# Kernel tuning notes

Hardware: AMD Instinct MI355X
Metric: run time of the kernel (lower is better)

## Reference

```python
import jax, jax.numpy as jnp
import numpy as np

V, D, H, L, S, B, FF, MAXLEN = 50257, 768, 12, 12, 1024, 4, 3072, 1024
HD = D // H
EPS = 1e-5


def layernorm(x, w, b):
    m = jnp.mean(x, axis=-1, keepdims=True)
    v = jnp.mean(jnp.square(x - m), axis=-1, keepdims=True)
    return (x - m) * jax.lax.rsqrt(v + EPS) * w + b


def setup_inputs() -> dict:
    key = jax.random.key(0)
    ks = jax.random.split(key, 8)
    std = 0.02
    return {
        "tokens": jax.random.randint(ks[0], (B, S), 0, V, dtype=jnp.int32),
        "wte": std * jax.random.normal(ks[1], (V, D), jnp.float32),
        "wpe": std * jax.random.normal(ks[2], (1, MAXLEN, D), jnp.float32),
        "ln1_w": jnp.ones((L, D), jnp.float32),
        "ln1_b": jnp.zeros((L, D), jnp.float32),
        "ln2_w": jnp.ones((L, D), jnp.float32),
        "ln2_b": jnp.zeros((L, D), jnp.float32),
        "W_exp": std * jax.random.normal(ks[3], (L, D, 3 * D), jnp.float32),
        "b_exp": jnp.zeros((L, 3 * D), jnp.float32),
        "W_o": std * jax.random.normal(ks[4], (L, D, D), jnp.float32),
        "b_o": jnp.zeros((L, D), jnp.float32),
        "W_ff1": std * jax.random.normal(ks[5], (L, D, FF), jnp.float32),
        "b_ff1": jnp.zeros((L, FF), jnp.float32),
        "W_ff2": std * jax.random.normal(ks[6], (L, FF, D), jnp.float32),
        "b_ff2": jnp.zeros((L, D), jnp.float32),
    }


def reference(tokens, wte, wpe, ln1_w, ln1_b, ln2_w, ln2_b,
              W_exp, b_exp, W_o, b_o, W_ff1, b_ff1, W_ff2, b_ff2):
    Bc, Sc = tokens.shape
    x = wte[tokens] + wpe[:, :Sc, :]                      # [B,S,D]
    mask = jnp.tril(jnp.ones((Sc, Sc), bool))             # causal (past=None)
    scale = 1.0 / jnp.sqrt(jnp.float32(HD))
    presents = []
    for l in range(L):
        h = layernorm(x, ln1_w[l], ln1_b[l])
        qkv = h @ W_exp[l] + b_exp[l]                     # [B,S,3D]
        q, k, v = jnp.split(qkv, 3, axis=-1)
        q = q.reshape(Bc, Sc, H, HD)
        k = k.reshape(Bc, Sc, H, HD)
        v = v.reshape(Bc, Sc, H, HD)
        presents.append(jnp.stack([k, v]))                # [2,B,S,H,HD]
        score = jnp.einsum('bqhd,bkhd->bhqk', q, k)
        score = jnp.where(mask, score, jnp.float32(-1e20))
        attn = jax.nn.softmax(score * scale, axis=-1)     # mask applied BEFORE scaling, as in source
        a = jnp.einsum('bhqk,bkhd->bqhd', attn, v).reshape(Bc, Sc, D)
        a = a @ W_o[l] + b_o[l]
        add = layernorm(a + x, ln2_w[l], ln2_b[l])        # LN2 on residual sum (GPT2-variant in source)
        ff = jax.nn.gelu(add @ W_ff1[l] + b_ff1[l], approximate=False)
        ff = ff @ W_ff2[l] + b_ff2[l]
        x = ff + add
    return x, jnp.stack(presents)                         # [L,2,B,S,H,HD]
```

## Files before the change

### kernel.cpp

```cpp
#include <hip/hip_runtime.h>
#include <hip/hip_bf16.h>
#include <math.h>

#define Bc 4
#define Sc 1024
#define Dc 768
#define Hc 12
#define Lc 12
#define FFc 3072
#define Mtot (Bc*Sc)

typedef __bf16 bf16x8 __attribute__((ext_vector_type(8)));
typedef float f32x4 __attribute__((ext_vector_type(4)));

__device__ __forceinline__ void gload_lds16(const void* g, void* l) {
    __builtin_amdgcn_global_load_lds((const __attribute__((address_space(1))) void*)g,
                                     (__attribute__((address_space(3))) void*)l, 16, 0, 0);
}

__global__ __launch_bounds__(256) void embed_kernel(const int* __restrict__ tokens,
                                                    const float* __restrict__ wte,
                                                    const float* __restrict__ wpe,
                                                    float* __restrict__ x) {
    int row = blockIdx.x;
    int s = row & (Sc - 1);
    int tok = tokens[row];
    const float* wt = wte + (size_t)tok * Dc;
    const float* wp = wpe + (size_t)s * Dc;
    float* xr = x + (size_t)row * Dc;
#pragma unroll
    for (int k = 0; k < 3; ++k) {
        int d = threadIdx.x + k * 256;
        xr[d] = wt[d] + wp[d];
    }
}

__global__ __launch_bounds__(256) void transpose_all_kernel(
        const float* __restrict__ We, const float* __restrict__ Wo,
        const float* __restrict__ Wf1, const float* __restrict__ Wf2,
        __bf16* __restrict__ Te, __bf16* __restrict__ To,
        __bf16* __restrict__ Tf1, __bf16* __restrict__ Tf2) {
    __shared__ float tl[32][33];
    int bid = blockIdx.x;
    const float* W; __bf16* T; int K, N, t;
    if (bid < 1728)      { W = We;  T = Te;  K = 768;  N = 2304; t = bid; }
    else if (bid < 2304) { W = Wo;  T = To;  K = 768;  N = 768;  t = bid - 1728; }
    else if (bid < 4608) { W = Wf1; T = Tf1; K = 768;  N = 3072; t = bid - 2304; }
    else                 { W = Wf2; T = Tf2; K = 3072; N = 768;  t = bid - 4608; }
    int nx = N >> 5;
    int n0 = (t % nx) * 32, k0 = (t / nx) * 32;
    int tx = threadIdx.x & 31, ty = threadIdx.x >> 5;
#pragma unroll
    for (int i = 0; i < 4; ++i)
        tl[ty + 8 * i][tx] = W[(size_t)(k0 + ty + 8 * i) * N + n0 + tx];
    __syncthreads();
#pragma unroll
    for (int i = 0; i < 4; ++i)
        T[(size_t)(n0 + ty + 8 * i) * K + k0 + tx] = (__bf16)tl[tx][ty + 8 * i];
}

template <bool DUAL>
__global__ __launch_bounds__(256) void ln_kernel(const float* __restrict__ x,
                                                 const float* __restrict__ lw,
                                                 const float* __restrict__ lb,
                                                 __bf16* __restrict__ outb,
                                                 float* __restrict__ outf) {
    int row = blockIdx.x;
    const float* xr = x + (size_t)row * Dc;
    int t = threadIdx.x;
    float v0 = xr[t], v1 = xr[t + 256], v2 = xr[t + 512];
    float s1 = v0 + v1 + v2;
    float s2 = v0 * v0 + v1 * v1 + v2 * v2;
    __shared__ float red[8];
#pragma unroll
    for (int o = 32; o; o >>= 1) {
        s1 += __shfl_down(s1, o);
        s2 += __shfl_down(s2, o);
    }
    int wv = t >> 6;
    if ((t & 63) == 0) { red[wv] = s1; red[4 + wv] = s2; }
    __syncthreads();
    float S1 = red[0] + red[1] + red[2] + red[3];
    float S2 = red[4] + red[5] + red[6] + red[7];
    float mean = S1 * (1.0f / Dc);
    float var = S2 * (1.0f / Dc) - mean * mean;
    float rs = rsqrtf(var + 1e-5f);
    size_t ro = (size_t)row * Dc;
    float o0 = (v0 - mean) * rs * lw[t]       + lb[t];
    float o1 = (v1 - mean) * rs * lw[t + 256] + lb[t + 256];
    float o2 = (v2 - mean) * rs * lw[t + 512] + lb[t + 512];
    outb[ro + t]       = (__bf16)o0;
    outb[ro + t + 256] = (__bf16)o1;
    outb[ro + t + 512] = (__bf16)o2;
    if (DUAL) {
        outf[ro + t]       = o0;
        outf[ro + t + 256] = o1;
        outf[ro + t + 512] = o2;
    }
}

template <int BMr, int BNc, int BK, int EPI>
__global__ __launch_bounds__(256) void gemm_bf16(const __bf16* __restrict__ A,
                                                 const __bf16* __restrict__ BT,
                                                 const float* __restrict__ bias,
                                                 const float* __restrict__ addin,
                                                 float* __restrict__ Cf,
                                                 __bf16* __restrict__ Cb,
                                                 float* __restrict__ pres,
                                                 int K, int N) {
    constexpr int HRm = BMr / 32, HRn = BNc / 32;
    constexpr int KS  = BK / 32;
    constexpr int LPR = BK / 8;
    constexpr int SSH = (BK == 32) ? 1 : 0;
    constexpr int IA  = BMr * BK / 2048;
    constexpr int IB  = BNc * BK / 2048;
    static_assert(IA * 2048 == BMr * BK && IB * 2048 == BNc * BK, "staging granularity");
    __shared__ __bf16 As[2][BMr * BK];
    __shared__ __bf16 Bs[2][BNc * BK];
    int tid = threadIdx.x;
    int w = tid >> 6, l = tid & 63;
    int wrow = (w >> 1) * (BMr / 2), wcol = (w & 1) * (BNc / 2);
    int brow0 = blockIdx.x * BMr, bcol0 = blockIdx.y * BNc;
    int rsel = l & 15, lg = l >> 4;

    f32x4 acc[HRm][HRn] = {};

    const __bf16* Abase = A + (size_t)brow0 * K;
    const __bf16* Bbase = BT + (size_t)bcol0 * K;

    auto stage = [&](int buf, int kt) {
#pragma unroll
        for (int i = 0; i < IA; ++i) {
            int cid = i * 256 + tid;
            int row = cid / LPR, slot = cid % LPR;
            int chunk = slot ^ ((row >> SSH) & (LPR - 1));
            gload_lds16(Abase + (size_t)row * K + kt + chunk * 8,
                        &As[buf][(i * 256 + w * 64) * 8]);
        }
#pragma unroll
        for (int i = 0; i < IB; ++i) {
            int cid = i * 256 + tid;
            int row = cid / LPR, slot = cid % LPR;
            int chunk = slot ^ ((row >> SSH) & (LPR - 1));
            gload_lds16(Bbase + (size_t)row * K + kt + chunk * 8,
                        &Bs[buf][(i * 256 + w * 64) * 8]);
        }
    };

    stage(0, 0);
    __syncthreads();
    int nk = K / BK;
    for (int kt = 0; kt < nk; ++kt) {
        int cur = kt & 1;
        if (kt + 1 < nk) stage(cur ^ 1, (kt + 1) * BK);
        bf16x8 af[KS][HRm], bfr[KS][HRn];
#pragma unroll
        for (int m = 0; m < HRm; ++m) {
            int r = wrow + m * 16 + rsel;
            int sw = (r >> SSH) & (LPR - 1);
#pragma unroll
            for (int s = 0; s < KS; ++s)
                af[s][m] = *(const bf16x8*)(&As[cur][r * BK + ((s * 4 + lg) ^ sw) * 8]);
        }
#pragma unroll
        for (int n = 0; n < HRn; ++n) {
            int r = wcol + n * 16 + rsel;
            int sw = (r >> SSH) & (LPR - 1);
#pragma unroll
            for (int s = 0; s < KS; ++s)
                bfr[s][n] = *(const bf16x8*)(&Bs[cur][r * BK + ((s * 4 + lg) ^ sw) * 8]);
        }
#pragma unroll
        for (int s = 0; s < KS; ++s)
#pragma unroll
            for (int m = 0; m < HRm; ++m)
#pragma unroll
                for (int n = 0; n < HRn; ++n)
                    acc[m][n] = __builtin_amdgcn_mfma_f32_16x16x32_bf16(af[s][m], bfr[s][n], acc[m][n], 0, 0, 0);
        __syncthreads();
    }

    int r4 = lg * 4, cc = rsel;
#pragma unroll
    for (int m = 0; m < HRm; ++m)
#pragma unroll
        for (int n = 0; n < HRn; ++n) {
            int col = bcol0 + wcol + n * 16 + cc;
            float bv = bias[col];
#pragma unroll
            for (int i = 0; i < 4; ++i) {
                int row = brow0 + wrow + m * 16 + r4 + i;
                float v = acc[m][n][i] + bv;
                if (EPI == 1) {
                    v += addin[(size_t)row * N + col];
                    Cf[(size_t)row * N + col] = v;
                }
                if (EPI == 2) {
                    float u = 0.7978845608f * (v + 0.044715f * v * v * v);
                    v = v / (1.0f + __expf(-2.0f * u));
                    Cb[(size_t)row * N + col] = (__bf16)v;
                }
                if (EPI == 3) {
                    Cb[(size_t)row * N + col] = (__bf16)v;
                    if (col >= 768) {
                        int kv = (col >= 1536) ? 1 : 0;
                        pres[((size_t)kv * Mtot + row) * Dc + (col - 768 - kv * 768)] = v;
                    }
                }
            }
        }
}

__global__ __launch_bounds__(256) void attn_mfma_kernel(const __bf16* __restrict__ qkvb,
                                                        __bf16* __restrict__ aout) {
    __shared__ __bf16 Ks[64 * 72];
    __shared__ __bf16 Vts[64 * 72];
    __shared__ __bf16 Ps[4][16 * 72];
    int bh = blockIdx.x;
    int b = bh / Hc, h = bh % Hc;
    int qt = (Sc / 64 - 1) - blockIdx.y;
    int tid = threadIdx.x;
    int w = tid >> 6, l = tid & 63;
    int lr = l & 15, lg = l >> 4;
    int qb = qt * 64;

    const __bf16* base = qkvb + (size_t)b * Sc * 2304 + h * 64;

    bf16x8 qf[2];
    {
        const __bf16* qrow = base + (size_t)(qb + w * 16 + lr) * 2304 + lg * 8;
        qf[0] = *(const bf16x8*)(qrow);
        qf[1] = *(const bf16x8*)(qrow + 32);
    }

    f32x4 O[4] = {};
    float mrow[4], lrowv[4];
#pragma unroll
    for (int i = 0; i < 4; ++i) { mrow[i] = -1e30f; lrowv[i] = 0.0f; }

    int kj = tid >> 2, kc = tid & 3;
    int vj = tid & 63, vd0 = (tid >> 6) * 8;

    for (int t = 0; t <= qt; ++t) {
        __syncthreads();
#pragma unroll
        for (int it = 0; it < 2; ++it) {
            int c = kc + 4 * it;
            bf16x8 v = *(const bf16x8*)(base + (size_t)(t * 64 + kj) * 2304 + 768 + c * 8);
            *(bf16x8*)(&Ks[kj * 72 + c * 8]) = v;
        }
#pragma unroll
        for (int it = 0; it < 2; ++it) {
            int d0 = vd0 + 32 * it;
            bf16x8 v = *(const bf16x8*)(base + (size_t)(t * 64 + vj) * 2304 + 1536 + d0);
#pragma unroll
            for (int i = 0; i < 8; ++i)
                Vts[(d0 + i) * 72 + vj] = v[i];
        }
        __syncthreads();

        f32x4 sc[4] = {};
        __builtin_amdgcn_s_setprio(1);
#pragma unroll
        for (int s = 0; s < 2; ++s)
#pragma unroll
            for (int n = 0; n < 4; ++n) {
                bf16x8 kf = *(const bf16x8*)(&Ks[(n * 16 + lr) * 72 + s * 32 + lg * 8]);
                sc[n] = __builtin_amdgcn_mfma_f32_16x16x32_bf16(qf[s], kf, sc[n], 0, 0, 0);
            }
        __builtin_amdgcn_s_setprio(0);

        bool diag = (t == qt);
#pragma unroll
        for (int n = 0; n < 4; ++n)
#pragma unroll
            for (int i = 0; i < 4; ++i) {
                float s = sc[n][i] * 0.125f;
                if (diag) {
                    int jg = n * 16 + lr;
                    int qg = w * 16 + lg * 4 + i;
                    if (jg > qg) s = -1e30f;
                }
                sc[n][i] = s;
            }
        float corr[4], psum[4];
#pragma unroll
        for (int i = 0; i < 4; ++i) {
            float mx = fmaxf(fmaxf(sc[0][i], sc[1][i]), fmaxf(sc[2][i], sc[3][i]));
#pragma unroll
            for (int o = 1; o < 16; o <<= 1) mx = fmaxf(mx, __shfl_xor(mx, o));
            float mnew = fmaxf(mrow[i], mx);
            corr[i] = __expf(mrow[i] - mnew);
            mrow[i] = mnew;
            psum[i] = 0.0f;
        }
#pragma unroll
        for (int n = 0; n < 4; ++n)
#pragma unroll
            for (int i = 0; i < 4; ++i) {
                float p = __expf(sc[n][i] - mrow[i]);
                psum[i] += p;
                Ps[w][(lg * 4 + i) * 72 + n * 16 + lr] = (__bf16)p;
            }
#pragma unroll
        for (int i = 0; i < 4; ++i) {
#pragma unroll
            for (int o = 1; o < 16; o <<= 1) psum[i] += __shfl_xor(psum[i], o);
            lrowv[i] = lrowv[i] * corr[i] + psum[i];
        }
#pragma unroll
        for (int n = 0; n < 4; ++n)
#pragma unroll
            for (int i = 0; i < 4; ++i) O[n][i] *= corr[i];
        __builtin_amdgcn_s_setprio(1);
#pragma unroll
        for (int s = 0; s < 2; ++s) {
            bf16x8 pf = *(const bf16x8*)(&Ps[w][lr * 72 + s * 32 + lg * 8]);
#pragma unroll
            for (int n = 0; n < 4; ++n) {
                bf16x8 vf = *(const bf16x8*)(&Vts[(n * 16 + lr) * 72 + s * 32 + lg * 8]);
                O[n] = __builtin_amdgcn_mfma_f32_16x16x32_bf16(pf, vf, O[n], 0, 0, 0);
            }
        }
        __builtin_amdgcn_s_setprio(0);
    }
    __bf16* orow = aout + (size_t)(b * Sc + qb + w * 16 + lg * 4) * Dc + h * 64 + lr;
#pragma unroll
    for (int n = 0; n < 4; ++n)
#pragma unroll
        for (int i = 0; i < 4; ++i)
            orow[(size_t)i * Dc + n * 16] = (__bf16)(O[n][i] / lrowv[i]);
}

extern "C" void kernel_launch(void* const* d_in, const int* in_sizes, int n_in,
                              void* d_out, int out_size, void* d_ws, size_t ws_size,
                              hipStream_t stream) {
    const int*   tokens = (const int*)d_in[0];
    const float* wte    = (const float*)d_in[1];
    const float* wpe    = (const float*)d_in[2];
    const float* ln1_w  = (const float*)d_in[3];
    const float* ln1_b  = (const float*)d_in[4];
    const float* ln2_w  = (const float*)d_in[5];
    const float* ln2_b  = (const float*)d_in[6];
    const float* W_exp  = (const float*)d_in[7];
    const float* b_exp  = (const float*)d_in[8];
    const float* W_o    = (const float*)d_in[9];
    const float* b_o    = (const float*)d_in[10];
    const float* W_ff1  = (const float*)d_in[11];
    const float* b_ff1  = (const float*)d_in[12];
    const float* W_ff2  = (const float*)d_in[13];
    const float* b_ff2  = (const float*)d_in[14];

    float* out_x    = (float*)d_out;
    float* out_pres = out_x + (size_t)Mtot * Dc;

    float* ws   = (float*)d_ws;
    float* x    = ws;
    float* addf = x + (size_t)Mtot * Dc;
    __bf16* hb   = (__bf16*)(addf + (size_t)Mtot * Dc);
    __bf16* addb = hb + (size_t)Mtot * Dc;
    __bf16* qkvb = addb + (size_t)Mtot * Dc;
    __bf16* ff1b = qkvb + (size_t)Mtot * 3 * Dc;
    __bf16* wt_exp = ff1b + (size_t)Mtot * FFc;
    __bf16* wt_o   = wt_exp + (size_t)2304 * 768;
    __bf16* wt_ff1 = wt_o   + (size_t)768 * 768;
    __bf16* wt_ff2 = wt_ff1 + (size_t)3072 * 768;

    embed_kernel<<<Mtot, 256, 0, stream>>>(tokens, wte, wpe, x);

    for (int lidx = 0; lidx < Lc; ++lidx) {
        transpose_all_kernel<<<6912, 256, 0, stream>>>(
            W_exp + (size_t)lidx * 768 * 2304, W_o + (size_t)lidx * 768 * 768,
            W_ff1 + (size_t)lidx * 768 * 3072, W_ff2 + (size_t)lidx * 3072 * 768,
            wt_exp, wt_o, wt_ff1, wt_ff2);

        ln_kernel<false><<<Mtot, 256, 0, stream>>>(
            x, ln1_w + lidx * Dc, ln1_b + lidx * Dc, hb, nullptr);
        gemm_bf16<64, 192, 32, 3><<<dim3(Mtot / 64, 2304 / 192), 256, 0, stream>>>(
            hb, wt_exp, b_exp + (size_t)lidx * 3 * Dc,
            nullptr, nullptr, qkvb, out_pres + (size_t)lidx * 2 * Mtot * Dc, 768, 2304);
        attn_mfma_kernel<<<dim3(Bc * Hc, Sc / 64), 256, 0, stream>>>(qkvb, hb);
        gemm_bf16<64, 96, 64, 1><<<dim3(Mtot / 64, 768 / 96), 256, 0, stream>>>(
            hb, wt_o, b_o + (size_t)lidx * Dc,
            x, x, nullptr, nullptr, 768, 768);
        ln_kernel<true><<<Mtot, 256, 0, stream>>>(
            x, ln2_w + lidx * Dc, ln2_b + lidx * Dc, addb, addf);
        gemm_bf16<128, 192, 32, 2><<<dim3(Mtot / 128, FFc / 192), 256, 0, stream>>>(
            addb, wt_ff1, b_ff1 + (size_t)lidx * FFc,
            nullptr, nullptr, ff1b, nullptr, 768, FFc);
        float* ff2dst = (lidx == Lc - 1) ? out_x : x;
        gemm_bf16<64, 96, 64, 1><<<dim3(Mtot / 64, 768 / 96), 256, 0, stream>>>(
            ff1b, wt_ff2, b_ff2 + (size_t)lidx * Dc,
            addf, ff2dst, nullptr, nullptr, 3072, 768);
    }
}
```

Measured before the change: 2.066 ms.

## Use bf16 residual intermediates, remap GEMM block order, enlarge FF2 tile

The attention-output GEMM now writes the residual sum as bf16, and LN2 reads that bf16 buffer and emits only a bf16 normalized output. The FF2 GEMM adds the bf16 LN2 output as its residual instead of a separate fp32 copy. This removes the fp32 addf buffer and its reads and writes. GEMM workgroups are also remapped with a stride-8 interleave meant for better cache and chiplet locality, and the FF2 GEMM moves to 128-row tiles. The cost is lower precision on the residual path, which can add numerical error.

```diff
diff --git a/kernel.cpp b/kernel.cpp
--- a/kernel.cpp
+++ b/kernel.cpp
@@ -59,16 +59,15 @@
         T[(size_t)(n0 + ty + 8 * i) * K + k0 + tx] = (__bf16)tl[tx][ty + 8 * i];
 }
 
-template <bool DUAL>
-__global__ __launch_bounds__(256) void ln_kernel(const float* __restrict__ x,
+template <typename TI>
+__global__ __launch_bounds__(256) void ln_kernel(const TI* __restrict__ x,
                                                  const float* __restrict__ lw,
                                                  const float* __restrict__ lb,
-                                                 __bf16* __restrict__ outb,
-                                                 float* __restrict__ outf) {
+                                                 __bf16* __restrict__ outb) {
     int row = blockIdx.x;
-    const float* xr = x + (size_t)row * Dc;
+    const TI* xr = x + (size_t)row * Dc;
     int t = threadIdx.x;
-    float v0 = xr[t], v1 = xr[t + 256], v2 = xr[t + 512];
+    float v0 = (float)xr[t], v1 = (float)xr[t + 256], v2 = (float)xr[t + 512];
     float s1 = v0 + v1 + v2;
     float s2 = v0 * v0 + v1 * v1 + v2 * v2;
     __shared__ float red[8];
@@ -86,24 +85,17 @@
     float var = S2 * (1.0f / Dc) - mean * mean;
     float rs = rsqrtf(var + 1e-5f);
     size_t ro = (size_t)row * Dc;
-    float o0 = (v0 - mean) * rs * lw[t]       + lb[t];
-    float o1 = (v1 - mean) * rs * lw[t + 256] + lb[t + 256];
-    float o2 = (v2 - mean) * rs * lw[t + 512] + lb[t + 512];
-    outb[ro + t]       = (__bf16)o0;
-    outb[ro + t + 256] = (__bf16)o1;
-    outb[ro + t + 512] = (__bf16)o2;
-    if (DUAL) {
-        outf[ro + t]       = o0;
-        outf[ro + t + 256] = o1;
-        outf[ro + t + 512] = o2;
-    }
+    outb[ro + t]       = (__bf16)((v0 - mean) * rs * lw[t]       + lb[t]);
+    outb[ro + t + 256] = (__bf16)((v1 - mean) * rs * lw[t + 256] + lb[t + 256]);
+    outb[ro + t + 512] = (__bf16)((v2 - mean) * rs * lw[t + 512] + lb[t + 512]);
 }
 
 template <int BMr, int BNc, int BK, int EPI>
 __global__ __launch_bounds__(256) void gemm_bf16(const __bf16* __restrict__ A,
                                                  const __bf16* __restrict__ BT,
                                                  const float* __restrict__ bias,
-                                                 const float* __restrict__ addin,
+                                                 const float* __restrict__ addf,
+                                                 const __bf16* __restrict__ addb,
                                                  float* __restrict__ Cf,
                                                  __bf16* __restrict__ Cb,
                                                  float* __restrict__ pres,
@@ -114,13 +106,19 @@
     constexpr int SSH = (BK == 32) ? 1 : 0;
     constexpr int IA  = BMr * BK / 2048;
     constexpr int IB  = BNc * BK / 2048;
+    constexpr int GXc = Mtot / BMr;
     static_assert(IA * 2048 == BMr * BK && IB * 2048 == BNc * BK, "staging granularity");
     __shared__ __bf16 As[2][BMr * BK];
     __shared__ __bf16 Bs[2][BNc * BK];
     int tid = threadIdx.x;
     int w = tid >> 6, l = tid & 63;
     int wrow = (w >> 1) * (BMr / 2), wcol = (w & 1) * (BNc / 2);
-    int brow0 = blockIdx.x * BMr, bcol0 = blockIdx.y * BNc;
+
+    int nwg = GXc * gridDim.y;
+    int lin = blockIdx.y * GXc + blockIdx.x;
+    int nl = (lin & 7) * (nwg >> 3) + (lin >> 3);
+    int brow0 = (nl % GXc) * BMr, bcol0 = (nl / GXc) * BNc;
+
     int rsel = l & 15, lg = l >> 4;
 
     f32x4 acc[HRm][HRn] = {};
@@ -191,10 +189,6 @@
             for (int i = 0; i < 4; ++i) {
                 int row = brow0 + wrow + m * 16 + r4 + i;
                 float v = acc[m][n][i] + bv;
-                if (EPI == 1) {
-                    v += addin[(size_t)row * N + col];
-                    Cf[(size_t)row * N + col] = v;
-                }
                 if (EPI == 2) {
                     float u = 0.7978845608f * (v + 0.044715f * v * v * v);
                     v = v / (1.0f + __expf(-2.0f * u));
@@ -206,6 +200,14 @@
                         int kv = (col >= 1536) ? 1 : 0;
                         pres[((size_t)kv * Mtot + row) * Dc + (col - 768 - kv * 768)] = v;
                     }
+                }
+                if (EPI == 4) {
+                    v += addf[(size_t)row * N + col];
+                    Cb[(size_t)row * N + col] = (__bf16)v;
+                }
+                if (EPI == 5) {
+                    v += (float)addb[(size_t)row * N + col];
+                    Cf[(size_t)row * N + col] = v;
                 }
             }
         }
@@ -356,9 +358,9 @@
 
     float* ws   = (float*)d_ws;
     float* x    = ws;
-    float* addf = x + (size_t)Mtot * Dc;
-    __bf16* hb   = (__bf16*)(addf + (size_t)Mtot * Dc);
-    __bf16* addb = hb + (size_t)Mtot * Dc;
+    __bf16* hb   = (__bf16*)(x + (size_t)Mtot * Dc);
+    __bf16* rb   = hb + (size_t)Mtot * Dc;
+    __bf16* addb = rb + (size_t)Mtot * Dc;
     __bf16* qkvb = addb + (size_t)Mtot * Dc;
     __bf16* ff1b = qkvb + (size_t)Mtot * 3 * Dc;
     __bf16* wt_exp = ff1b + (size_t)Mtot * FFc;
@@ -374,23 +376,24 @@
             W_ff1 + (size_t)lidx * 768 * 3072, W_ff2 + (size_t)lidx * 3072 * 768,
             wt_exp, wt_o, wt_ff1, wt_ff2);
 
-        ln_kernel<false><<<Mtot, 256, 0, stream>>>(
-            x, ln1_w + lidx * Dc, ln1_b + lidx * Dc, hb, nullptr);
+        ln_kernel<float><<<Mtot, 256, 0, stream>>>(
+            x, ln1_w + lidx * Dc, ln1_b + lidx * Dc, hb);
         gemm_bf16<64, 192, 32, 3><<<dim3(Mtot / 64, 2304 / 192), 256, 0, stream>>>(
             hb, wt_exp, b_exp + (size_t)lidx * 3 * Dc,
-            nullptr, nullptr, qkvb, out_pres + (size_t)lidx * 2 * Mtot * Dc, 768, 2304);
+            nullptr, nullptr, nullptr, qkvb,
+            out_pres + (size_t)lidx * 2 * Mtot * Dc, 768, 2304);
         attn_mfma_kernel<<<dim3(Bc * Hc, Sc / 64), 256, 0, stream>>>(qkvb, hb);
-        gemm_bf16<64, 96, 64, 1><<<dim3(Mtot / 64, 768 / 96), 256, 0, stream>>>(
+        gemm_bf16<64, 96, 64, 4><<<dim3(Mtot / 64, 768 / 96), 256, 0, stream>>>(
             hb, wt_o, b_o + (size_t)lidx * Dc,
-            x, x, nullptr, nullptr, 768, 768);
-        ln_kernel<true><<<Mtot, 256, 0, stream>>>(
-            x, ln2_w + lidx * Dc, ln2_b + lidx * Dc, addb, addf);
+            x, nullptr, nullptr, rb, nullptr, 768, 768);
+        ln_kernel<__bf16><<<Mtot, 256, 0, stream>>>(
+            rb, ln2_w + lidx * Dc, ln2_b + lidx * Dc, addb);
         gemm_bf16<128, 192, 32, 2><<<dim3(Mtot / 128, FFc / 192), 256, 0, stream>>>(
             addb, wt_ff1, b_ff1 + (size_t)lidx * FFc,
-            nullptr, nullptr, ff1b, nullptr, 768, FFc);
+            nullptr, nullptr, nullptr, ff1b, nullptr, 768, FFc);
         float* ff2dst = (lidx == Lc - 1) ? out_x : x;
-        gemm_bf16<64, 96, 64, 1><<<dim3(Mtot / 64, 768 / 96), 256, 0, stream>>>(
+        gemm_bf16<128, 96, 64, 5><<<dim3(Mtot / 128, 768 / 96), 256, 0, stream>>>(
             ff1b, wt_ff2, b_ff2 + (size_t)lidx * Dc,
-            addf, ff2dst, nullptr, nullptr, 3072, 768);
-    }
-}
+            nullptr, addb, ff2dst, nullptr, nullptr, 3072, 768);
+    }
+}
```

After: 2.189 ms. +6.0%, slower.
